# Kernel tuning notes

Measured on AMD Instinct MI355X. Metric: run time of the kernel, lower is better.

## Reference

```python
import jax, jax.numpy as jnp
import numpy as np

N, B, E = 10000, 4, 160000
C_IN, C_OUT, C_E = 64, 64, 16


def _mk_params(key, c_in, c_out, c_e):
    ks = jax.random.split(key, 8)
    s = 0.1
    return dict(
        w_n=jax.random.normal(ks[0], (c_in, c_out), jnp.float32) * s,
        w_e=jax.random.normal(ks[1], (c_e, c_out), jnp.float32) * s,
        q=jax.random.normal(ks[2], (c_out, c_out), jnp.float32) * s,
        k=jax.random.normal(ks[3], (c_out, c_out), jnp.float32) * s,
        aw=jax.random.normal(ks[4], (3 * c_out, 1), jnp.float32) * s,
        ab=jax.random.normal(ks[5], (1,), jnp.float32) * s,
        ow=jax.random.normal(ks[6], (2 * c_out, c_out), jnp.float32) * s,
        ob=jax.random.normal(ks[7], (c_out,), jnp.float32) * s,
    )


def setup_inputs() -> dict:
    key = jax.random.key(0)
    kx, ke, ka, k1, k2 = jax.random.split(key, 5)
    inp = {
        'X': jax.random.normal(kx, (N, B, C_IN), jnp.float32),
        'edge_index': jax.random.randint(ke, (2, E), 0, N, jnp.int32),
        'edge_attr': jax.random.normal(ka, (E, C_E), jnp.float32),
    }
    p1 = _mk_params(k1, C_IN, C_OUT, C_E)
    p2 = _mk_params(k2, C_OUT, C_OUT, C_E)
    for name, v in p1.items():
        inp[name + '1'] = v
    for name, v in p2.items():
        inp[name + '2'] = v
    return inp


def egnn_conv(x, edge_index, edge_attr, w_n, w_e, q, k, aw, ab, ow, ob, n_nodes):
    # x: [N,B,Cin]; edge_attr: [E,Ce]
    xp = x @ w_n                         # [N,B,C]
    ea = edge_attr @ w_e                 # [E,C]
    src, dst = edge_index[0], edge_index[1]
    xj = xp[src]                         # [E,B,C] gather (source)
    xi = xp[dst]                         # [E,B,C] gather (target)
    qf = xj @ q                          # [E,B,C]
    kf = xi @ k                          # [E,B,C]
    eab = jnp.broadcast_to(ea[:, None, :], qf.shape)  # [E,B,C]
    att_feat = jnp.concatenate([qf, kf, eab], axis=-1)  # [E,B,3C]
    att = jax.nn.sigmoid(att_feat @ aw + ab)            # [E,B,1]
    gate = jax.nn.sigmoid(eab)
    msg = att * xj * gate                # [E,B,C]
    aggr = jax.ops.segment_max(msg, dst, num_segments=n_nodes)  # [N,B,C]
    aggr = jnp.where(jnp.isneginf(aggr), 0.0, aggr)  # empty segments -> 0
    out = jnp.concatenate([xp, aggr], axis=-1) @ ow + ob
    return xp + out


def reference(X, edge_index, edge_attr,
              w_n1, w_e1, q1, k1, aw1, ab1, ow1, ob1,
              w_n2, w_e2, q2, k2, aw2, ab2, ow2, ob2):
    n_nodes = X.shape[0]
    c1 = egnn_conv(X, edge_index, edge_attr, w_n1, w_e1, q1, k1, aw1, ab1, ow1, ob1, n_nodes)
    c1 = jax.nn.leaky_relu(c1, 0.01)
    c2 = egnn_conv(c1, edge_index, edge_attr, w_n2, w_e2, q2, k2, aw2, ab2, ow2, ob2, n_nodes)
    c2 = jax.nn.leaky_relu(c2, 0.01)
    return c2
```

## Files before the change

### kernel.cpp

```cpp
#include <hip/hip_runtime.h>
#include <math.h>

#define NN 10000
#define BB 4
#define EE 160000
#define CC 64
#define CE 16

static constexpr size_t OFF_XPA    = 0;
static constexpr size_t OFF_XPB    = 10240000;
static constexpr size_t OFF_SA     = 20480000;
static constexpr size_t OFF_SB     = 20640000;
static constexpr size_t OFF_VECS   = 20800000;
static constexpr size_t OFF_COUNTS = 20801280;
static constexpr size_t OFF_CURSOR = 20841280;
static constexpr size_t OFF_OFFS   = 20881280;
static constexpr size_t OFF_RECS   = 20921344;
static constexpr size_t OFF_ATT    = 22201344;

__device__ __forceinline__ float sigmoidf_(float x) {
    return 1.0f / (1.0f + __expf(-x));
}

__global__ void hist_vecs_kernel(const int* __restrict__ ei, int* __restrict__ counts,
                                 const float* __restrict__ q1, const float* __restrict__ k1,
                                 const float* __restrict__ aw1, const float* __restrict__ we1,
                                 const float* __restrict__ q2, const float* __restrict__ k2,
                                 const float* __restrict__ aw2, const float* __restrict__ we2,
                                 float* __restrict__ vecs) {
    int e = blockIdx.x * blockDim.x + threadIdx.x;
    if (e < EE) atomicAdd(&counts[ei[EE + e]], 1);
    if (blockIdx.x == 0) {
        int t = threadIdx.x;
        if (t < 64) {
            float a = 0.f, b = 0.f, c = 0.f, d = 0.f;
            for (int j = 0; j < 64; ++j) {
                a = fmaf(q1[t * 64 + j], aw1[j], a);
                b = fmaf(k1[t * 64 + j], aw1[64 + j], b);
                c = fmaf(q2[t * 64 + j], aw2[j], c);
                d = fmaf(k2[t * 64 + j], aw2[64 + j], d);
            }
            vecs[t] = a; vecs[64 + t] = b; vecs[144 + t] = c; vecs[208 + t] = d;
        }
        if (t < 16) {
            float a = 0.f, b = 0.f;
            for (int j = 0; j < 64; ++j) {
                a = fmaf(we1[t * 64 + j], aw1[128 + j], a);
                b = fmaf(we2[t * 64 + j], aw2[128 + j], b);
            }
            vecs[128 + t] = a; vecs[272 + t] = b;
        }
    }
}

__global__ void scan_kernel(const int* __restrict__ counts, int* __restrict__ offs, int n) {
    __shared__ int sm[1024];
    __shared__ int carry_s;
    int t = threadIdx.x;
    if (t == 0) carry_s = 0;
    __syncthreads();
    for (int base = 0; base < n; base += 1024) {
        int i = base + t;
        int v = (i < n) ? counts[i] : 0;
        sm[t] = v;
        __syncthreads();
        for (int off = 1; off < 1024; off <<= 1) {
            int add = (t >= off) ? sm[t - off] : 0;
            __syncthreads();
            sm[t] += add;
            __syncthreads();
        }
        int carry = carry_s;
        if (i < n) offs[i] = carry + sm[t] - v;
        __syncthreads();
        if (t == 1023) carry_s = carry + sm[1023];
        __syncthreads();
    }
    if (t == 0) offs[n] = carry_s;
}

__global__ void scatter_kernel(const int* __restrict__ ei, const int* __restrict__ offs,
                               int* __restrict__ cursor, int2* __restrict__ recs) {
    int e = blockIdx.x * blockDim.x + threadIdx.x;
    if (e >= EE) return;
    int s = ei[e], d = ei[EE + e];
    int p = atomicAdd(&cursor[d], 1);
    recs[offs[d] + p] = make_int2(s, e);
}

__global__ __launch_bounds__(256) void node_prep_kernel(
    const float* __restrict__ x,
    const float* __restrict__ w_n,
    const float* __restrict__ qa,
    const float* __restrict__ ka,
    float* __restrict__ xp,
    float* __restrict__ sa,
    float* __restrict__ sb) {
    __shared__ float w_sh[64 * 64];
    __shared__ float x_sh[4 * BB * CC];
    int t = threadIdx.x;
    for (int i = t; i < 64 * 64; i += 256) w_sh[i] = w_n[i];
    int node0 = blockIdx.x * 4;
    const float4* xg = (const float4*)(x + (size_t)node0 * BB * CC);
    ((float4*)x_sh)[t] = xg[t];
    __syncthreads();
    int wave = t >> 6, lane = t & 63;
    int node = node0 + wave;
    const float* xrow = x_sh + wave * BB * CC;
    float acc0 = 0.f, acc1 = 0.f, acc2 = 0.f, acc3 = 0.f;
    #pragma unroll 8
    for (int ci = 0; ci < 64; ++ci) {
        float w = w_sh[ci * 64 + lane];
        acc0 = fmaf(xrow[ci], w, acc0);
        acc1 = fmaf(xrow[64 + ci], w, acc1);
        acc2 = fmaf(xrow[128 + ci], w, acc2);
        acc3 = fmaf(xrow[192 + ci], w, acc3);
    }
    size_t obase = (size_t)node * BB * CC + lane;
    xp[obase] = acc0;
    xp[obase + 64] = acc1;
    xp[obase + 128] = acc2;
    xp[obase + 192] = acc3;
    float qv = qa[lane], kv = ka[lane];
    float ra0 = acc0 * qv, ra1 = acc1 * qv, ra2 = acc2 * qv, ra3 = acc3 * qv;
    float rb0 = acc0 * kv, rb1 = acc1 * kv, rb2 = acc2 * kv, rb3 = acc3 * kv;
    #pragma unroll
    for (int off = 32; off >= 1; off >>= 1) {
        ra0 += __shfl_xor(ra0, off, 64); ra1 += __shfl_xor(ra1, off, 64);
        ra2 += __shfl_xor(ra2, off, 64); ra3 += __shfl_xor(ra3, off, 64);
        rb0 += __shfl_xor(rb0, off, 64); rb1 += __shfl_xor(rb1, off, 64);
        rb2 += __shfl_xor(rb2, off, 64); rb3 += __shfl_xor(rb3, off, 64);
    }
    if (lane == 0) {
        sa[node * BB + 0] = ra0; sa[node * BB + 1] = ra1;
        sa[node * BB + 2] = ra2; sa[node * BB + 3] = ra3;
        sb[node * BB + 0] = rb0; sb[node * BB + 1] = rb1;
        sb[node * BB + 2] = rb2; sb[node * BB + 3] = rb3;
    }
}

__global__ __launch_bounds__(256) void att_kernel(
    const int* __restrict__ ei, const float* __restrict__ attr,
    const float* __restrict__ sa, const float* __restrict__ sb,
    const float* __restrict__ weav,
    const float* __restrict__ ab,
    float4* __restrict__ att) {
    int e = blockIdx.x * blockDim.x + threadIdx.x;
    if (e >= EE) return;
    int s = ei[e], d = ei[EE + e];
    const float4* ap = (const float4*)(attr + (size_t)e * CE);
    float4 a0 = ap[0], a1 = ap[1], a2 = ap[2], a3 = ap[3];
    float se = ab[0];
    se = fmaf(a0.x, weav[0], se);  se = fmaf(a0.y, weav[1], se);
    se = fmaf(a0.z, weav[2], se);  se = fmaf(a0.w, weav[3], se);
    se = fmaf(a1.x, weav[4], se);  se = fmaf(a1.y, weav[5], se);
    se = fmaf(a1.z, weav[6], se);  se = fmaf(a1.w, weav[7], se);
    se = fmaf(a2.x, weav[8], se);  se = fmaf(a2.y, weav[9], se);
    se = fmaf(a2.z, weav[10], se); se = fmaf(a2.w, weav[11], se);
    se = fmaf(a3.x, weav[12], se); se = fmaf(a3.y, weav[13], se);
    se = fmaf(a3.z, weav[14], se); se = fmaf(a3.w, weav[15], se);
    float4 sas = *(const float4*)(sa + (size_t)s * BB);
    float4 sbn = *(const float4*)(sb + (size_t)d * BB);
    float4 r;
    r.x = sigmoidf_(sas.x + sbn.x + se);
    r.y = sigmoidf_(sas.y + sbn.y + se);
    r.z = sigmoidf_(sas.z + sbn.z + se);
    r.w = sigmoidf_(sas.w + sbn.w + se);
    att[e] = r;
}

__global__ __launch_bounds__(256) void conv_out_kernel(
    const float* __restrict__ xp,
    const int2* __restrict__ recs,
    const int* __restrict__ offs,
    const float* __restrict__ attr,
    const float* __restrict__ w_e,
    const float4* __restrict__ att,
    const float* __restrict__ ow,
    const float* __restrict__ ob,
    float* __restrict__ out) {
    __shared__ float aggr_sh[4][BB * CC];
    __shared__ float xpn_sh[4][BB * CC];
    int t = threadIdx.x;
    int wave = t >> 6, lane = t & 63;
    int node = blockIdx.x * 4 + wave;

    float wec[CE];
    #pragma unroll
    for (int j = 0; j < CE; ++j) wec[j] = w_e[j * CC + lane];

    const float* xn = xp + (size_t)node * BB * CC + lane;
    float xn0 = xn[0], xn1 = xn[64], xn2 = xn[128], xn3 = xn[192];

    int o0 = offs[node], o1 = offs[node + 1];
    float m0 = -INFINITY, m1 = -INFINITY, m2 = -INFINITY, m3 = -INFINITY;

    int i = o0;
    int2 rec = (i < o1) ? recs[i] : make_int2(0, 0);
    while (i < o1) {
        int2 cur = rec;
        ++i;
        if (i < o1) rec = recs[i];
        int s = cur.x, e = cur.y;
        float4 at = att[e];
        const float4* ap = (const float4*)(attr + (size_t)e * CE);
        float4 a0 = ap[0], a1 = ap[1], a2 = ap[2], a3 = ap[3];
        float g = 0.f;
        g = fmaf(a0.x, wec[0], g);  g = fmaf(a0.y, wec[1], g);
        g = fmaf(a0.z, wec[2], g);  g = fmaf(a0.w, wec[3], g);
        g = fmaf(a1.x, wec[4], g);  g = fmaf(a1.y, wec[5], g);
        g = fmaf(a1.z, wec[6], g);  g = fmaf(a1.w, wec[7], g);
        g = fmaf(a2.x, wec[8], g);  g = fmaf(a2.y, wec[9], g);
        g = fmaf(a2.z, wec[10], g); g = fmaf(a2.w, wec[11], g);
        g = fmaf(a3.x, wec[12], g); g = fmaf(a3.y, wec[13], g);
        g = fmaf(a3.z, wec[14], g); g = fmaf(a3.w, wec[15], g);
        g = sigmoidf_(g);
        const float* xs = xp + (size_t)s * BB * CC + lane;
        float x0 = xs[0], x1 = xs[64], x2 = xs[128], x3 = xs[192];
        m0 = fmaxf(m0, at.x * x0 * g);
        m1 = fmaxf(m1, at.y * x1 * g);
        m2 = fmaxf(m2, at.z * x2 * g);
        m3 = fmaxf(m3, at.w * x3 * g);
    }
    m0 = (m0 == -INFINITY) ? 0.f : m0;
    m1 = (m1 == -INFINITY) ? 0.f : m1;
    m2 = (m2 == -INFINITY) ? 0.f : m2;
    m3 = (m3 == -INFINITY) ? 0.f : m3;

    aggr_sh[wave][0 * CC + lane] = m0; aggr_sh[wave][1 * CC + lane] = m1;
    aggr_sh[wave][2 * CC + lane] = m2; aggr_sh[wave][3 * CC + lane] = m3;
    xpn_sh[wave][0 * CC + lane] = xn0; xpn_sh[wave][1 * CC + lane] = xn1;
    xpn_sh[wave][2 * CC + lane] = xn2; xpn_sh[wave][3 * CC + lane] = xn3;
    __syncthreads();

    const float* xr = xpn_sh[wave];
    const float* ar = aggr_sh[wave];
    float o0f = 0.f, o1f = 0.f, o2f = 0.f, o3f = 0.f;
    #pragma unroll 4
    for (int ci = 0; ci < 64; ++ci) {
        float wa = ow[ci * 64 + lane];
        float wb = ow[(64 + ci) * 64 + lane];
        o0f = fmaf(xr[ci], wa, o0f);
        o1f = fmaf(xr[CC + ci], wa, o1f);
        o2f = fmaf(xr[2 * CC + ci], wa, o2f);
        o3f = fmaf(xr[3 * CC + ci], wa, o3f);
        o0f = fmaf(ar[ci], wb, o0f);
        o1f = fmaf(ar[CC + ci], wb, o1f);
        o2f = fmaf(ar[2 * CC + ci], wb, o2f);
        o3f = fmaf(ar[3 * CC + ci], wb, o3f);
    }
    float obv = ob[lane];
    float r0 = xn0 + o0f + obv;
    float r1 = xn1 + o1f + obv;
    float r2 = xn2 + o2f + obv;
    float r3 = xn3 + o3f + obv;
    r0 = (r0 > 0.f) ? r0 : 0.01f * r0;
    r1 = (r1 > 0.f) ? r1 : 0.01f * r1;
    r2 = (r2 > 0.f) ? r2 : 0.01f * r2;
    r3 = (r3 > 0.f) ? r3 : 0.01f * r3;
    float* op = out + (size_t)node * BB * CC + lane;
    op[0] = r0; op[64] = r1; op[128] = r2; op[192] = r3;
}

extern "C" void kernel_launch(void* const* d_in, const int* in_sizes, int n_in,
                              void* d_out, int out_size, void* d_ws, size_t ws_size,
                              hipStream_t stream) {
    const float* X    = (const float*)d_in[0];
    const int*   ei   = (const int*)d_in[1];
    const float* attr = (const float*)d_in[2];
    const float* w_n1 = (const float*)d_in[3];
    const float* w_e1 = (const float*)d_in[4];
    const float* q1   = (const float*)d_in[5];
    const float* k1   = (const float*)d_in[6];
    const float* aw1  = (const float*)d_in[7];
    const float* ab1  = (const float*)d_in[8];
    const float* ow1  = (const float*)d_in[9];
    const float* ob1  = (const float*)d_in[10];
    const float* w_n2 = (const float*)d_in[11];
    const float* w_e2 = (const float*)d_in[12];
    const float* q2   = (const float*)d_in[13];
    const float* k2   = (const float*)d_in[14];
    const float* aw2  = (const float*)d_in[15];
    const float* ab2  = (const float*)d_in[16];
    const float* ow2  = (const float*)d_in[17];
    const float* ob2  = (const float*)d_in[18];
    float* out = (float*)d_out;

    char* ws = (char*)d_ws;
    float*  xpA    = (float*)(ws + OFF_XPA);
    float*  xpB    = (float*)(ws + OFF_XPB);
    float*  sa     = (float*)(ws + OFF_SA);
    float*  sb     = (float*)(ws + OFF_SB);
    float*  vecs   = (float*)(ws + OFF_VECS);
    int*    counts = (int*)(ws + OFF_COUNTS);
    int*    cursor = (int*)(ws + OFF_CURSOR);
    int*    offs   = (int*)(ws + OFF_OFFS);
    int2*   recs   = (int2*)(ws + OFF_RECS);
    float4* att    = (float4*)(ws + OFF_ATT);

    hipMemsetAsync(counts, 0, 2 * NN * sizeof(int), stream);
    hist_vecs_kernel<<<EE / 256, 256, 0, stream>>>(ei, counts, q1, k1, aw1, w_e1,
                                                   q2, k2, aw2, w_e2, vecs);
    scan_kernel<<<1, 1024, 0, stream>>>(counts, offs, NN);
    scatter_kernel<<<EE / 256, 256, 0, stream>>>(ei, offs, cursor, recs);

    node_prep_kernel<<<NN / 4, 256, 0, stream>>>(X, w_n1, vecs + 0, vecs + 64, xpA, sa, sb);
    att_kernel<<<EE / 256, 256, 0, stream>>>(ei, attr, sa, sb, vecs + 128, ab1, att);
    conv_out_kernel<<<NN / 4, 256, 0, stream>>>(xpA, recs, offs, attr, w_e1, att,
                                                ow1, ob1, xpB);
    node_prep_kernel<<<NN / 4, 256, 0, stream>>>(xpB, w_n2, vecs + 144, vecs + 208, xpA, sa, sb);
    att_kernel<<<EE / 256, 256, 0, stream>>>(ei, attr, sa, sb, vecs + 272, ab2, att);
    conv_out_kernel<<<NN / 4, 256, 0, stream>>>(xpA, recs, offs, attr, w_e2, att,
                                                ow2, ob2, out);
}
```

Baseline: 309.6 us.

## Degree-sort nodes for conv load balance, precompute edge scores, faster scan

Adds an order kernel that counting-sorts nodes by in-degree, descending, so conv_out blocks process nodes of similar degree and waves within a block finish together. Both layers' edge-attribute attention terms are computed once in the scatter kernel and stored, so att_kernel no longer rereads edge_attr. The single-block scan is rewritten as a per-thread serial plus wave-shuffle scan, the sigmoid uses a hardware reciprocal, and the block barrier in conv_out is replaced by an LDS wait, since each wave only reads its own shared slice. Costs are an extra tiny kernel and indirect node indexing.

```diff
diff --git a/kernel.cpp b/kernel.cpp
--- a/kernel.cpp
+++ b/kernel.cpp
@@ -17,9 +17,11 @@
 static constexpr size_t OFF_OFFS   = 20881280;
 static constexpr size_t OFF_RECS   = 20921344;
 static constexpr size_t OFF_ATT    = 22201344;
+static constexpr size_t OFF_SE12   = 24761344;
+static constexpr size_t OFF_ORDER  = 26041344;
 
 __device__ __forceinline__ float sigmoidf_(float x) {
-    return 1.0f / (1.0f + __expf(-x));
+    return __builtin_amdgcn_rcpf(1.0f + __expf(-x));
 }
 
 __global__ void hist_vecs_kernel(const int* __restrict__ ei, int* __restrict__ counts,
@@ -53,39 +55,119 @@
     }
 }
 
-__global__ void scan_kernel(const int* __restrict__ counts, int* __restrict__ offs, int n) {
-    __shared__ int sm[1024];
-    __shared__ int carry_s;
+__global__ __launch_bounds__(1024) void scan_kernel(const int* __restrict__ counts,
+                                                    int* __restrict__ offs, int n) {
+    __shared__ int wsum[16];
     int t = threadIdx.x;
-    if (t == 0) carry_s = 0;
-    __syncthreads();
-    for (int base = 0; base < n; base += 1024) {
-        int i = base + t;
-        int v = (i < n) ? counts[i] : 0;
-        sm[t] = v;
-        __syncthreads();
-        for (int off = 1; off < 1024; off <<= 1) {
-            int add = (t >= off) ? sm[t - off] : 0;
-            __syncthreads();
-            sm[t] += add;
-            __syncthreads();
+    int base = t * 10;
+    int v[10];
+    int s = 0;
+    #pragma unroll
+    for (int j = 0; j < 10; ++j) {
+        int i = base + j;
+        v[j] = (i < n) ? counts[i] : 0;
+        s += v[j];
+    }
+    int lane = t & 63, wid = t >> 6;
+    int ps = s;
+    #pragma unroll
+    for (int off = 1; off < 64; off <<= 1) {
+        int u = __shfl_up(ps, off, 64);
+        if (lane >= off) ps += u;
+    }
+    if (lane == 63) wsum[wid] = ps;
+    __syncthreads();
+    int wbase = 0;
+    for (int w = 0; w < wid; ++w) wbase += wsum[w];
+    int tb = wbase + ps - s;
+    #pragma unroll
+    for (int j = 0; j < 10; ++j) {
+        int i = base + j;
+        if (i < n) offs[i] = tb;
+        tb += v[j];
+    }
+    if (t == 1023) offs[n] = tb;
+}
+
+__global__ __launch_bounds__(1024) void order_kernel(const int* __restrict__ counts,
+                                                     int* __restrict__ order) {
+    __shared__ int hist[1024];
+    __shared__ int startb[1024];
+    __shared__ int cur[1024];
+    __shared__ int wsum[16];
+    int t = threadIdx.x;
+    hist[t] = 0; cur[t] = 0;
+    __syncthreads();
+    int dg[10];
+    #pragma unroll
+    for (int j = 0; j < 10; ++j) {
+        int i = t * 10 + j;
+        dg[j] = -1;
+        if (i < NN) {
+            int d = counts[i];
+            d = (d > 1023) ? 1023 : d;
+            dg[j] = d;
+            atomicAdd(&hist[d], 1);
         }
-        int carry = carry_s;
-        if (i < n) offs[i] = carry + sm[t] - v;
-        __syncthreads();
-        if (t == 1023) carry_s = carry + sm[1023];
-        __syncthreads();
-    }
-    if (t == 0) offs[n] = carry_s;
-}
-
-__global__ void scatter_kernel(const int* __restrict__ ei, const int* __restrict__ offs,
-                               int* __restrict__ cursor, int2* __restrict__ recs) {
+    }
+    __syncthreads();
+    int r = 1023 - t;
+    int v = hist[r];
+    int lane = t & 63, wid = t >> 6;
+    int ps = v;
+    #pragma unroll
+    for (int off = 1; off < 64; off <<= 1) {
+        int u = __shfl_up(ps, off, 64);
+        if (lane >= off) ps += u;
+    }
+    if (lane == 63) wsum[wid] = ps;
+    __syncthreads();
+    int wbase = 0;
+    for (int w = 0; w < wid; ++w) wbase += wsum[w];
+    startb[r] = wbase + ps - v;
+    __syncthreads();
+    #pragma unroll
+    for (int j = 0; j < 10; ++j) {
+        if (dg[j] >= 0) {
+            int pos = startb[dg[j]] + atomicAdd(&cur[dg[j]], 1);
+            order[pos] = t * 10 + j;
+        }
+    }
+}
+
+__global__ __launch_bounds__(256) void scatter_kernel(
+    const int* __restrict__ ei, const int* __restrict__ offs,
+    int* __restrict__ cursor, const float* __restrict__ attr,
+    const float* __restrict__ vecs, const float* __restrict__ ab1,
+    const float* __restrict__ ab2, int2* __restrict__ recs,
+    float2* __restrict__ se12) {
     int e = blockIdx.x * blockDim.x + threadIdx.x;
     if (e >= EE) return;
     int s = ei[e], d = ei[EE + e];
+    const float4* ap = (const float4*)(attr + (size_t)e * CE);
+    float4 a0 = ap[0], a1 = ap[1], a2 = ap[2], a3 = ap[3];
+    const float* v1 = vecs + 128;
+    const float* v2 = vecs + 272;
+    float s1 = ab1[0], s2 = ab2[0];
+    s1 = fmaf(a0.x, v1[0], s1);  s1 = fmaf(a0.y, v1[1], s1);
+    s1 = fmaf(a0.z, v1[2], s1);  s1 = fmaf(a0.w, v1[3], s1);
+    s1 = fmaf(a1.x, v1[4], s1);  s1 = fmaf(a1.y, v1[5], s1);
+    s1 = fmaf(a1.z, v1[6], s1);  s1 = fmaf(a1.w, v1[7], s1);
+    s1 = fmaf(a2.x, v1[8], s1);  s1 = fmaf(a2.y, v1[9], s1);
+    s1 = fmaf(a2.z, v1[10], s1); s1 = fmaf(a2.w, v1[11], s1);
+    s1 = fmaf(a3.x, v1[12], s1); s1 = fmaf(a3.y, v1[13], s1);
+    s1 = fmaf(a3.z, v1[14], s1); s1 = fmaf(a3.w, v1[15], s1);
+    s2 = fmaf(a0.x, v2[0], s2);  s2 = fmaf(a0.y, v2[1], s2);
+    s2 = fmaf(a0.z, v2[2], s2);  s2 = fmaf(a0.w, v2[3], s2);
+    s2 = fmaf(a1.x, v2[4], s2);  s2 = fmaf(a1.y, v2[5], s2);
+    s2 = fmaf(a1.z, v2[6], s2);  s2 = fmaf(a1.w, v2[7], s2);
+    s2 = fmaf(a2.x, v2[8], s2);  s2 = fmaf(a2.y, v2[9], s2);
+    s2 = fmaf(a2.z, v2[10], s2); s2 = fmaf(a2.w, v2[11], s2);
+    s2 = fmaf(a3.x, v2[12], s2); s2 = fmaf(a3.y, v2[13], s2);
+    s2 = fmaf(a3.z, v2[14], s2); s2 = fmaf(a3.w, v2[15], s2);
     int p = atomicAdd(&cursor[d], 1);
     recs[offs[d] + p] = make_int2(s, e);
+    se12[e] = make_float2(s1, s2);
 }
 
 __global__ __launch_bounds__(256) void node_prep_kernel(
@@ -140,25 +222,14 @@
 }
 
 __global__ __launch_bounds__(256) void att_kernel(
-    const int* __restrict__ ei, const float* __restrict__ attr,
+    const int* __restrict__ ei, const float2* __restrict__ se12,
     const float* __restrict__ sa, const float* __restrict__ sb,
-    const float* __restrict__ weav,
-    const float* __restrict__ ab,
-    float4* __restrict__ att) {
+    float4* __restrict__ att, int sel) {
     int e = blockIdx.x * blockDim.x + threadIdx.x;
     if (e >= EE) return;
     int s = ei[e], d = ei[EE + e];
-    const float4* ap = (const float4*)(attr + (size_t)e * CE);
-    float4 a0 = ap[0], a1 = ap[1], a2 = ap[2], a3 = ap[3];
-    float se = ab[0];
-    se = fmaf(a0.x, weav[0], se);  se = fmaf(a0.y, weav[1], se);
-    se = fmaf(a0.z, weav[2], se);  se = fmaf(a0.w, weav[3], se);
-    se = fmaf(a1.x, weav[4], se);  se = fmaf(a1.y, weav[5], se);
-    se = fmaf(a1.z, weav[6], se);  se = fmaf(a1.w, weav[7], se);
-    se = fmaf(a2.x, weav[8], se);  se = fmaf(a2.y, weav[9], se);
-    se = fmaf(a2.z, weav[10], se); se = fmaf(a2.w, weav[11], se);
-    se = fmaf(a3.x, weav[12], se); se = fmaf(a3.y, weav[13], se);
-    se = fmaf(a3.z, weav[14], se); se = fmaf(a3.w, weav[15], se);
+    float2 se2 = se12[e];
+    float se = sel ? se2.y : se2.x;
     float4 sas = *(const float4*)(sa + (size_t)s * BB);
     float4 sbn = *(const float4*)(sb + (size_t)d * BB);
     float4 r;
@@ -178,12 +249,13 @@
     const float4* __restrict__ att,
     const float* __restrict__ ow,
     const float* __restrict__ ob,
+    const int* __restrict__ order,
     float* __restrict__ out) {
     __shared__ float aggr_sh[4][BB * CC];
     __shared__ float xpn_sh[4][BB * CC];
     int t = threadIdx.x;
     int wave = t >> 6, lane = t & 63;
-    int node = blockIdx.x * 4 + wave;
+    int node = order[blockIdx.x * 4 + wave];
 
     float wec[CE];
     #pragma unroll
@@ -231,7 +303,7 @@
     aggr_sh[wave][2 * CC + lane] = m2; aggr_sh[wave][3 * CC + lane] = m3;
     xpn_sh[wave][0 * CC + lane] = xn0; xpn_sh[wave][1 * CC + lane] = xn1;
     xpn_sh[wave][2 * CC + lane] = xn2; xpn_sh[wave][3 * CC + lane] = xn3;
-    __syncthreads();
+    asm volatile("s_waitcnt lgkmcnt(0)" ::: "memory");
 
     const float* xr = xpn_sh[wave];
     const float* ar = aggr_sh[wave];
@@ -297,19 +369,22 @@
     int*    offs   = (int*)(ws + OFF_OFFS);
     int2*   recs   = (int2*)(ws + OFF_RECS);
     float4* att    = (float4*)(ws + OFF_ATT);
+    float2* se12   = (float2*)(ws + OFF_SE12);
+    int*    order  = (int*)(ws + OFF_ORDER);
 
     hipMemsetAsync(counts, 0, 2 * NN * sizeof(int), stream);
     hist_vecs_kernel<<<EE / 256, 256, 0, stream>>>(ei, counts, q1, k1, aw1, w_e1,
                                                    q2, k2, aw2, w_e2, vecs);
     scan_kernel<<<1, 1024, 0, stream>>>(counts, offs, NN);
-    scatter_kernel<<<EE / 256, 256, 0, stream>>>(ei, offs, cursor, recs);
-
+    order_kernel<<<1, 1024, 0, stream>>>(counts, order);
+    scatter_kernel<<<EE / 256, 256, 0, stream>>>(ei, offs, cursor, attr, vecs,
+                                                 ab1, ab2, recs, se12);
     node_prep_kernel<<<NN / 4, 256, 0, stream>>>(X, w_n1, vecs + 0, vecs + 64, xpA, sa, sb);
-    att_kernel<<<EE / 256, 256, 0, stream>>>(ei, attr, sa, sb, vecs + 128, ab1, att);
+    att_kernel<<<EE / 256, 256, 0, stream>>>(ei, se12, sa, sb, att, 0);
     conv_out_kernel<<<NN / 4, 256, 0, stream>>>(xpA, recs, offs, attr, w_e1, att,
-                                                ow1, ob1, xpB);
+                                                ow1, ob1, order, xpB);
     node_prep_kernel<<<NN / 4, 256, 0, stream>>>(xpB, w_n2, vecs + 144, vecs + 208, xpA, sa, sb);
-    att_kernel<<<EE / 256, 256, 0, stream>>>(ei, attr, sa, sb, vecs + 272, ab2, att);
+    att_kernel<<<EE / 256, 256, 0, stream>>>(ei, se12, sa, sb, att, 1);
     conv_out_kernel<<<NN / 4, 256, 0, stream>>>(xpA, recs, offs, attr, w_e2, att,
-                                                ow2, ob2, out);
-}
+                                                ow2, ob2, order, out);
+}
```

Result: faster. 289.6 us (-6.4%).
